# Performance work log

Measured on AMD Instinct MI355X. Metric: run time of the kernel, lower is better.

The kernel has to match this reference:

```python
import jax, jax.numpy as jnp
import numpy as np

CUTOFF = 10.0
EPS_W = 1e-5
EPS_LN = 1e-5

def _silu(v):
    return v * jax.nn.sigmoid(v)

def setup_inputs() -> dict:
    key = jax.random.key(0)
    ks = jax.random.split(key, 12)
    N, E, H, R = 50000, 300000, 256, 64
    s = lambda fan_in: 1.0 / np.sqrt(fan_in)
    inp = {
        'x': jax.random.normal(ks[0], (N, H), jnp.float32),
        'edge_index': jax.random.randint(ks[1], (2, E), 0, N, jnp.int64 if jax.config.jax_enable_x64 else jnp.int32),
        'distances': jax.random.uniform(ks[2], (E,), jnp.float32) * CUTOFF,
        'centers': jnp.linspace(0.0, CUTOFF, R).astype(jnp.float32),
        'widths': jnp.full((R,), CUTOFF / R, jnp.float32),
        'rbf_w1': jax.random.normal(ks[3], (R, R), jnp.float32) * s(R),
        'rbf_b1': jnp.zeros((R,), jnp.float32),
        'rbf_w2': jax.random.normal(ks[4], (R, R), jnp.float32) * s(R),
        'rbf_b2': jnp.zeros((R,), jnp.float32),
        'filt_w1': jax.random.normal(ks[5], (R, H), jnp.float32) * s(R),
        'filt_b1': jnp.zeros((H,), jnp.float32),
        'filt_w2': jax.random.normal(ks[6], (H, H), jnp.float32) * s(H),
        'filt_b2': jnp.zeros((H,), jnp.float32),
        'filt_w3': jax.random.normal(ks[7], (H, H), jnp.float32) * s(H),
        'filt_b3': jnp.zeros((H,), jnp.float32),
        'node_w': jax.random.normal(ks[8], (H, H), jnp.float32) * s(H),
        'node_b': jnp.zeros((H,), jnp.float32),
        'ln_g': jnp.ones((H,), jnp.float32),
        'ln_b': jnp.zeros((H,), jnp.float32),
        'gate_w': jax.random.normal(ks[9], (H, H), jnp.float32) * s(H),
        'gate_b': jnp.zeros((H,), jnp.float32),
    }
    return inp

def reference(x, edge_index, distances, centers, widths,
              rbf_w1, rbf_b1, rbf_w2, rbf_b2,
              filt_w1, filt_b1, filt_w2, filt_b2, filt_w3, filt_b3,
              node_w, node_b, ln_g, ln_b, gate_w, gate_b):
    # LearnableRBF: envelope * gaussian basis, then 2-layer SiLU proj
    d = distances
    env = 0.5 * (jnp.cos(d * jnp.pi / CUTOFF) + 1.0) * (d < CUTOFF).astype(x.dtype)  # [E]
    rbf = jnp.exp(-0.5 * ((d[:, None] - centers) / (jnp.abs(widths) + EPS_W)) ** 2)   # [E,R]
    r = rbf * env[:, None]
    r = _silu(r @ rbf_w1 + rbf_b1) @ rbf_w2 + rbf_b2                                  # [E,R]
    # filter network: Lin-SiLU-Lin-SiLU-Lin
    W = _silu(r @ filt_w1 + filt_b1)
    W = _silu(W @ filt_w2 + filt_b2) @ filt_w3 + filt_b3                              # [E,H]
    # gather -> modulate -> scatter-add (CFConv messaging)
    row, col = edge_index[0], edge_index[1]
    msg = (x[col] @ node_w + node_b) * W                                              # [E,H]
    agg = jax.ops.segment_sum(msg, row, num_segments=x.shape[0])                      # [N,H]
    h = x + agg
    mu = jnp.mean(h, axis=-1, keepdims=True)
    var = jnp.var(h, axis=-1, keepdims=True)
    out = (h - mu) / jnp.sqrt(var + EPS_LN) * ln_g + ln_b
    return out * jax.nn.sigmoid(out @ gate_w + gate_b)
```

## Files before the change

### kernel.cpp

```cpp
#include <hip/hip_runtime.h>
#include <hip/hip_bf16.h>
#include <math.h>

typedef __attribute__((ext_vector_type(8))) short bf16x8;
typedef __attribute__((ext_vector_type(4))) float f32x4;
typedef unsigned short ushort_t;

constexpr float F_CUTOFF = 10.0f;
constexpr float F_EPS_W  = 1e-5f;
constexpr float F_EPS_LN = 1e-5f;
constexpr float F_PI     = 3.14159265358979323846f;

__device__ __forceinline__ float silu_f(float v)   { return v / (1.0f + __expf(-v)); }
__device__ __forceinline__ float sigmoid_f(float v){ return 1.0f / (1.0f + __expf(-v)); }

__device__ __forceinline__ ushort_t f2bf(float f) {
    union { __hip_bfloat16 h; ushort_t u; } v; v.h = __float2bfloat16(f); return v.u;
}
__device__ __forceinline__ float bf2f(ushort_t u) {
    union { __hip_bfloat16 h; ushort_t u; } v; v.u = u; return __bfloat162float(v.h);
}

__device__ __forceinline__ float f4c(const float4& v, int q) {
    return q == 0 ? v.x : q == 1 ? v.y : q == 2 ? v.z : v.w;
}

__global__ void cvt_transpose_kernel(const float* __restrict__ in, ushort_t* __restrict__ out,
                                     int K, int N, int logK)
{
    int idx = blockIdx.x * 256 + threadIdx.x;
    if (idx >= K * N) return;
    int n = idx >> logK;
    int k = idx & (K - 1);
    out[idx] = f2bf(in[k * N + n]);
}

__global__ __launch_bounds__(256)
void gemm256_bf16_kernel(const float* __restrict__ A, const float* __restrict__ Wm,
                         const float* __restrict__ bias, ushort_t* __restrict__ out, int M)
{
    __shared__ float4 As4[64][64];
    const int t = threadIdx.x;
    const int row0 = blockIdx.x * 64;

    #pragma unroll
    for (int i = 0; i < 16; ++i) {
        int flat = t + i * 256;
        int r = flat >> 6, k4 = flat & 63;
        int row = row0 + r;
        float4 v = make_float4(0.f, 0.f, 0.f, 0.f);
        if (row < M) v = reinterpret_cast<const float4*>(A)[row * 64 + k4];
        As4[r][k4] = v;
    }
    __syncthreads();

    const int jt  = t & 31;
    const int et  = t >> 5;
    const int j04 = jt * 2;
    const int r0  = et * 8;

    float acc[8][8];
    #pragma unroll
    for (int r = 0; r < 8; ++r)
        #pragma unroll
        for (int c = 0; c < 8; ++c) acc[r][c] = 0.f;

    for (int k4 = 0; k4 < 64; ++k4) {
        float4 a4[8];
        #pragma unroll
        for (int r = 0; r < 8; ++r) a4[r] = As4[r0 + r][k4];
        #pragma unroll
        for (int q = 0; q < 4; ++q) {
            const int k = k4 * 4 + q;
            float4 b0 = reinterpret_cast<const float4*>(Wm)[k * 64 + j04];
            float4 b1 = reinterpret_cast<const float4*>(Wm)[k * 64 + j04 + 1];
            float bb[8] = {b0.x, b0.y, b0.z, b0.w, b1.x, b1.y, b1.z, b1.w};
            #pragma unroll
            for (int r = 0; r < 8; ++r) {
                float av = f4c(a4[r], q);
                #pragma unroll
                for (int c = 0; c < 8; ++c) acc[r][c] = fmaf(av, bb[c], acc[r][c]);
            }
        }
    }

    float4 bv0 = reinterpret_cast<const float4*>(bias)[j04];
    float4 bv1 = reinterpret_cast<const float4*>(bias)[j04 + 1];
    float bb[8] = {bv0.x, bv0.y, bv0.z, bv0.w, bv1.x, bv1.y, bv1.z, bv1.w};

    #pragma unroll
    for (int r = 0; r < 8; ++r) {
        int row = row0 + r0 + r;
        if (row >= M) continue;
        ushort_t o8[8];
        #pragma unroll
        for (int c = 0; c < 8; ++c) o8[c] = f2bf(acc[r][c] + bb[c]);
        *reinterpret_cast<uint4*>(out + (size_t)row * 256 + jt * 8) = *reinterpret_cast<uint4*>(o8);
    }
}

__global__ __launch_bounds__(256)
void gate_gemm_kernel(const float* __restrict__ A, const float* __restrict__ Wm,
                      const float* __restrict__ bias, float* __restrict__ out, int M)
{
    __shared__ float4 As4[64][64];
    const int t = threadIdx.x;
    const int row0 = blockIdx.x * 64;

    #pragma unroll
    for (int i = 0; i < 16; ++i) {
        int flat = t + i * 256;
        int r = flat >> 6, k4 = flat & 63;
        int row = row0 + r;
        float4 v = make_float4(0.f, 0.f, 0.f, 0.f);
        if (row < M) v = reinterpret_cast<const float4*>(A)[row * 64 + k4];
        As4[r][k4] = v;
    }
    __syncthreads();

    const int jt  = t & 31;
    const int et  = t >> 5;
    const int j04 = jt * 2;
    const int r0  = et * 8;

    float acc[8][8];
    #pragma unroll
    for (int r = 0; r < 8; ++r)
        #pragma unroll
        for (int c = 0; c < 8; ++c) acc[r][c] = 0.f;

    for (int k4 = 0; k4 < 64; ++k4) {
        float4 a4[8];
        #pragma unroll
        for (int r = 0; r < 8; ++r) a4[r] = As4[r0 + r][k4];
        #pragma unroll
        for (int q = 0; q < 4; ++q) {
            const int k = k4 * 4 + q;
            float4 b0 = reinterpret_cast<const float4*>(Wm)[k * 64 + j04];
            float4 b1 = reinterpret_cast<const float4*>(Wm)[k * 64 + j04 + 1];
            float bb[8] = {b0.x, b0.y, b0.z, b0.w, b1.x, b1.y, b1.z, b1.w};
            #pragma unroll
            for (int r = 0; r < 8; ++r) {
                float av = f4c(a4[r], q);
                #pragma unroll
                for (int c = 0; c < 8; ++c) acc[r][c] = fmaf(av, bb[c], acc[r][c]);
            }
        }
    }

    float4 bv0 = reinterpret_cast<const float4*>(bias)[j04];
    float4 bv1 = reinterpret_cast<const float4*>(bias)[j04 + 1];
    float bb[8] = {bv0.x, bv0.y, bv0.z, bv0.w, bv1.x, bv1.y, bv1.z, bv1.w};

    #pragma unroll
    for (int r = 0; r < 8; ++r) {
        int row = row0 + r0 + r;
        if (row >= M) continue;
        float4 a0 = As4[r0 + r][j04];
        float4 a1 = As4[r0 + r][j04 + 1];
        float aa[8] = {a0.x, a0.y, a0.z, a0.w, a1.x, a1.y, a1.z, a1.w};
        float o[8];
        #pragma unroll
        for (int c = 0; c < 8; ++c) o[c] = aa[c] * sigmoid_f(acc[r][c] + bb[c]);
        reinterpret_cast<float4*>(out)[row * 64 + j04]     = make_float4(o[0], o[1], o[2], o[3]);
        reinterpret_cast<float4*>(out)[row * 64 + j04 + 1] = make_float4(o[4], o[5], o[6], o[7]);
    }
}

template<int KS, int NT, bool SILU>
__device__ __forceinline__ void mlp_stage(const unsigned char* in, unsigned char* out,
                                          const ushort_t* __restrict__ Wt,
                                          const float* __restrict__ bias,
                                          int wm, int wn, int g, int q)
{
    constexpr int K = KS * 32;
    f32x4 acc[4][NT];
    #pragma unroll
    for (int mt = 0; mt < 4; ++mt)
        #pragma unroll
        for (int nt = 0; nt < NT; ++nt) acc[mt][nt] = (f32x4){0.f, 0.f, 0.f, 0.f};

    #pragma unroll
    for (int kk = 0; kk < KS; ++kk) {
        bf16x8 a[4];
        #pragma unroll
        for (int mt = 0; mt < 4; ++mt) {
            int m = wm * 64 + mt * 16 + q;
            int unit = (4 * kk + g) ^ (m & 7);
            a[mt] = *reinterpret_cast<const bf16x8*>(in + m * 512 + unit * 16);
        }
        bf16x8 b[NT];
        #pragma unroll
        for (int nt = 0; nt < NT; ++nt) {
            int n = (wn * NT + nt) * 16 + q;
            b[nt] = *reinterpret_cast<const bf16x8*>(Wt + n * K + kk * 32 + g * 8);
        }
        #pragma unroll
        for (int mt = 0; mt < 4; ++mt)
            #pragma unroll
            for (int nt = 0; nt < NT; ++nt)
                acc[mt][nt] = __builtin_amdgcn_mfma_f32_16x16x32_bf16(a[mt], b[nt], acc[mt][nt], 0, 0, 0);
    }

    const bool evenq = (q & 1) == 0;
    #pragma unroll
    for (int nt = 0; nt < NT; ++nt) {
        int n0  = (wn * NT + nt) * 16 + q;
        int n_e = n0 & ~1;
        float2 bv = *reinterpret_cast<const float2*>(bias + n_e);
        #pragma unroll
        for (int mt = 0; mt < 4; ++mt) {
            float v[4], p[4];
            #pragma unroll
            for (int r = 0; r < 4; ++r) { v[r] = acc[mt][nt][r]; p[r] = __shfl_xor(v[r], 1, 64); }
            #pragma unroll
            for (int rr = 0; rr < 2; ++rr) {
                int r = evenq ? rr : (2 + rr);
                float lo = (evenq ? v[r] : p[r]) + bv.x;
                float hi = (evenq ? p[r] : v[r]) + bv.y;
                if (SILU) { lo = silu_f(lo); hi = silu_f(hi); }
                int m = wm * 64 + mt * 16 + 4 * g + r;
                unsigned u = (unsigned)f2bf(lo) | ((unsigned)f2bf(hi) << 16);
                int byte = m * 512 + (((n_e >> 3) ^ (m & 7)) << 4) + ((n_e & 7) * 2);
                *reinterpret_cast<unsigned*>(out + byte) = u;
            }
        }
    }
}

__global__ __launch_bounds__(512)
void edge_mfma_kernel(const float* __restrict__ dist, const int* __restrict__ eidx,
                      const float* __restrict__ centers, const float* __restrict__ widths,
                      const ushort_t* __restrict__ wt_rbf1, const float* __restrict__ rbf_b1,
                      const ushort_t* __restrict__ wt_rbf2, const float* __restrict__ rbf_b2,
                      const ushort_t* __restrict__ wt_f1, const float* __restrict__ filt_b1,
                      const ushort_t* __restrict__ wt_f2, const float* __restrict__ filt_b2,
                      const ushort_t* __restrict__ wt_f3, const float* __restrict__ filt_b3,
                      const ushort_t* __restrict__ y, float* __restrict__ agg, int E)
{
    extern __shared__ __align__(16) unsigned char smem[];
    unsigned char* bufA = smem;
    unsigned char* bufB = smem + 65536;

    const int t  = threadIdx.x;
    const int e0 = blockIdx.x * 128;
    const int w    = t >> 6;
    const int wm   = w >> 2, wn = w & 3;
    const int lane = t & 63;
    const int g = lane >> 4, q = lane & 15;

    {
        int e  = t >> 2;
        int k0 = (t & 3) * 16;
        int ge = e0 + e;
        float d = (ge < E) ? dist[ge] : F_CUTOFF;
        float env = (d < F_CUTOFF) ? 0.5f * (__cosf(d * (F_PI / F_CUTOFF)) + 1.0f) : 0.0f;
        unsigned char* rowp = bufA + e * 512;
        #pragma unroll
        for (int i = 0; i < 8; ++i) {
            int n = k0 + 2 * i;
            float c0 = centers[n],     w0 = fabsf(widths[n]) + F_EPS_W;
            float c1 = centers[n + 1], w1 = fabsf(widths[n + 1]) + F_EPS_W;
            float z0 = (d - c0) / w0, z1 = (d - c1) / w1;
            float r0 = env * __expf(-0.5f * z0 * z0);
            float r1 = env * __expf(-0.5f * z1 * z1);
            unsigned u = (unsigned)f2bf(r0) | ((unsigned)f2bf(r1) << 16);
            int byte = (((n >> 3) ^ (e & 7)) << 4) + ((n & 7) * 2);
            *reinterpret_cast<unsigned*>(rowp + byte) = u;
        }
    }
    __syncthreads();

    mlp_stage<2, 1, true >(bufA, bufB, wt_rbf1, rbf_b1, wm, wn, g, q);
    __syncthreads();
    mlp_stage<2, 1, false>(bufB, bufA, wt_rbf2, rbf_b2, wm, wn, g, q);
    __syncthreads();
    mlp_stage<2, 4, true >(bufA, bufB, wt_f1, filt_b1, wm, wn, g, q);
    __syncthreads();
    mlp_stage<8, 4, true >(bufB, bufA, wt_f2, filt_b2, wm, wn, g, q);
    __syncthreads();

    {
        f32x4 acc[4][4];
        #pragma unroll
        for (int mt = 0; mt < 4; ++mt)
            #pragma unroll
            for (int nt = 0; nt < 4; ++nt) acc[mt][nt] = (f32x4){0.f, 0.f, 0.f, 0.f};

        #pragma unroll
        for (int kk = 0; kk < 8; ++kk) {
            bf16x8 a[4];
            #pragma unroll
            for (int mt = 0; mt < 4; ++mt) {
                int m = wm * 64 + mt * 16 + q;
                int unit = (4 * kk + g) ^ (m & 7);
                a[mt] = *reinterpret_cast<const bf16x8*>(bufA + m * 512 + unit * 16);
            }
            bf16x8 b[4];
            #pragma unroll
            for (int nt = 0; nt < 4; ++nt) {
                int n = (wn * 4 + nt) * 16 + q;
                b[nt] = *reinterpret_cast<const bf16x8*>(wt_f3 + n * 256 + kk * 32 + g * 8);
            }
            #pragma unroll
            for (int mt = 0; mt < 4; ++mt)
                #pragma unroll
                for (int nt = 0; nt < 4; ++nt)
                    acc[mt][nt] = __builtin_amdgcn_mfma_f32_16x16x32_bf16(a[mt], b[nt], acc[mt][nt], 0, 0, 0);
        }

        float bn[4];
        int   nn[4];
        #pragma unroll
        for (int nt = 0; nt < 4; ++nt) { nn[nt] = (wn * 4 + nt) * 16 + q; bn[nt] = filt_b3[nn[nt]]; }

        #pragma unroll
        for (int mt = 0; mt < 4; ++mt) {
            #pragma unroll
            for (int r = 0; r < 4; ++r) {
                int m  = wm * 64 + mt * 16 + 4 * g + r;
                int ge = e0 + m;
                if (ge < E) {
                    int rowi = eidx[ge];
                    int coli = eidx[E + ge];
                    const ushort_t* yrow = y + (size_t)coli * 256;
                    float* arow = agg + (size_t)rowi * 256;
                    #pragma unroll
                    for (int nt = 0; nt < 4; ++nt) {
                        float wv = acc[mt][nt][r] + bn[nt];
                        float yv = bf2f(yrow[nn[nt]]);
                        unsafeAtomicAdd(&arow[nn[nt]], wv * yv);
                    }
                }
            }
        }
    }
}

__global__ __launch_bounds__(256)
void ln_kernel(const float* __restrict__ x, const float* __restrict__ agg,
               const float* __restrict__ g, const float* __restrict__ b,
               float* __restrict__ out0, int N)
{
    int lane = threadIdx.x & 63;
    int row  = blockIdx.x * 4 + (threadIdx.x >> 6);
    if (row >= N) return;
    float4 hx = reinterpret_cast<const float4*>(x)[row * 64 + lane];
    float4 ha = reinterpret_cast<const float4*>(agg)[row * 64 + lane];
    float4 h  = make_float4(hx.x + ha.x, hx.y + ha.y, hx.z + ha.z, hx.w + ha.w);
    float s  = h.x + h.y + h.z + h.w;
    float s2 = h.x * h.x + h.y * h.y + h.z * h.z + h.w * h.w;
    #pragma unroll
    for (int off = 32; off > 0; off >>= 1) {
        s  += __shfl_xor(s,  off, 64);
        s2 += __shfl_xor(s2, off, 64);
    }
    float mu  = s * (1.0f / 256.0f);
    float var = s2 * (1.0f / 256.0f) - mu * mu;
    float inv = rsqrtf(var + F_EPS_LN);
    float4 gv = reinterpret_cast<const float4*>(g)[lane];
    float4 bv = reinterpret_cast<const float4*>(b)[lane];
    float4 o;
    o.x = (h.x - mu) * inv * gv.x + bv.x;
    o.y = (h.y - mu) * inv * gv.y + bv.y;
    o.z = (h.z - mu) * inv * gv.z + bv.z;
    o.w = (h.w - mu) * inv * gv.w + bv.w;
    reinterpret_cast<float4*>(out0)[row * 64 + lane] = o;
}

extern "C" void kernel_launch(void* const* d_in, const int* in_sizes, int n_in,
                              void* d_out, int out_size, void* d_ws, size_t ws_size,
                              hipStream_t stream)
{
    const float* x       = (const float*)d_in[0];
    const int*   eidx    = (const int*)  d_in[1];
    const float* dist    = (const float*)d_in[2];
    const float* centers = (const float*)d_in[3];
    const float* widths  = (const float*)d_in[4];
    const float* rbf_w1  = (const float*)d_in[5];
    const float* rbf_b1  = (const float*)d_in[6];
    const float* rbf_w2  = (const float*)d_in[7];
    const float* rbf_b2  = (const float*)d_in[8];
    const float* filt_w1 = (const float*)d_in[9];
    const float* filt_b1 = (const float*)d_in[10];
    const float* filt_w2 = (const float*)d_in[11];
    const float* filt_b2 = (const float*)d_in[12];
    const float* filt_w3 = (const float*)d_in[13];
    const float* filt_b3 = (const float*)d_in[14];
    const float* node_w  = (const float*)d_in[15];
    const float* node_b  = (const float*)d_in[16];
    const float* ln_g    = (const float*)d_in[17];
    const float* ln_b    = (const float*)d_in[18];
    const float* gate_w  = (const float*)d_in[19];
    const float* gate_b  = (const float*)d_in[20];

    const int N = in_sizes[0] / 256;
    const int E = in_sizes[2];

    ushort_t* y_bf = (ushort_t*)d_ws;
    ushort_t* wt1  = y_bf + (size_t)N * 256;
    ushort_t* wt2  = wt1 + 64 * 64;
    ushort_t* wf1  = wt2 + 64 * 64;
    ushort_t* wf2  = wf1 + 256 * 64;
    ushort_t* wf3  = wf2 + 256 * 256;

    float* agg = (float*)d_out;

    hipMemsetAsync(d_out, 0, (size_t)out_size * sizeof(float), stream);

    cvt_transpose_kernel<<<dim3((64 * 64 + 255) / 256),   256, 0, stream>>>(rbf_w1,  wt1, 64, 64, 6);
    cvt_transpose_kernel<<<dim3((64 * 64 + 255) / 256),   256, 0, stream>>>(rbf_w2,  wt2, 64, 64, 6);
    cvt_transpose_kernel<<<dim3((64 * 256 + 255) / 256),  256, 0, stream>>>(filt_w1, wf1, 64, 256, 6);
    cvt_transpose_kernel<<<dim3((256 * 256 + 255) / 256), 256, 0, stream>>>(filt_w2, wf2, 256, 256, 8);
    cvt_transpose_kernel<<<dim3((256 * 256 + 255) / 256), 256, 0, stream>>>(filt_w3, wf3, 256, 256, 8);

    gemm256_bf16_kernel<<<dim3((N + 63) / 64), 256, 0, stream>>>(x, node_w, node_b, y_bf, N);

    hipFuncSetAttribute((const void*)edge_mfma_kernel,
                        hipFuncAttributeMaxDynamicSharedMemorySize, 131072);
    edge_mfma_kernel<<<dim3((E + 127) / 128), 512, 131072, stream>>>(
        dist, eidx, centers, widths,
        wt1, rbf_b1, wt2, rbf_b2,
        wf1, filt_b1, wf2, filt_b2, wf3, filt_b3,
        y_bf, agg, E);

    ln_kernel<<<dim3((N + 3) / 4), 256, 0, stream>>>(x, agg, ln_g, ln_b, (float*)d_out, N);
    gate_gemm_kernel<<<dim3((N + 63) / 64), 256, 0, stream>>>((float*)d_out, gate_w, gate_b, (float*)d_out, N);
}
```

Baseline: 1.022 ms.

## Fold rbf_w2 into filt_w1 and halve edge tile for higher occupancy

Since the second RBF layer has no activation, its weight and bias are precomputed into the first filter layer (W2·Wf1, b2·Wf1+bf1) by small prep kernels. This removes one MFMA stage and one block-wide barrier per edge tile. The edge tile also shrinks from 128 to 64 edges, so shared memory drops to 64KB static with launch bounds requesting 4 blocks, aiming for more resident blocks to hide gather and atomic latency. The trade-off is that the fused weight is rounded to bf16 after combining, which changes rounding slightly, and each block now reuses the loaded weights over fewer edges.

Result: faster. 848.0 us (-17.1%).

```diff
diff --git a/kernel.cpp b/kernel.cpp
--- a/kernel.cpp
+++ b/kernel.cpp
@@ -33,6 +33,27 @@
     int n = idx >> logK;
     int k = idx & (K - 1);
     out[idx] = f2bf(in[k * N + n]);
+}
+
+__global__ void combine_w_kernel(const float* __restrict__ w2, const float* __restrict__ fw1,
+                                 ushort_t* __restrict__ out)
+{
+    int idx = blockIdx.x * 256 + threadIdx.x;
+    int c = idx >> 6, j = idx & 63;
+    float s = 0.f;
+    #pragma unroll 8
+    for (int n = 0; n < 64; ++n) s += w2[j * 64 + n] * fw1[n * 256 + c];
+    out[idx] = f2bf(s);
+}
+
+__global__ void combine_b_kernel(const float* __restrict__ b2, const float* __restrict__ fw1,
+                                 const float* __restrict__ fb1, float* __restrict__ out)
+{
+    int c = threadIdx.x;
+    float s = fb1[c];
+    #pragma unroll 8
+    for (int n = 0; n < 64; ++n) s += b2[n] * fw1[n * 256 + c];
+    out[c] = s;
 }
 
 __global__ __launch_bounds__(256)
@@ -174,29 +195,29 @@
                                           int wm, int wn, int g, int q)
 {
     constexpr int K = KS * 32;
-    f32x4 acc[4][NT];
-    #pragma unroll
-    for (int mt = 0; mt < 4; ++mt)
+    f32x4 acc[2][NT];
+    #pragma unroll
+    for (int mt = 0; mt < 2; ++mt)
         #pragma unroll
         for (int nt = 0; nt < NT; ++nt) acc[mt][nt] = (f32x4){0.f, 0.f, 0.f, 0.f};
 
     #pragma unroll
     for (int kk = 0; kk < KS; ++kk) {
-        bf16x8 a[4];
-        #pragma unroll
-        for (int mt = 0; mt < 4; ++mt) {
-            int m = wm * 64 + mt * 16 + q;
-            int unit = (4 * kk + g) ^ (m & 7);
-            a[mt] = *reinterpret_cast<const bf16x8*>(in + m * 512 + unit * 16);
-        }
         bf16x8 b[NT];
         #pragma unroll
         for (int nt = 0; nt < NT; ++nt) {
             int n = (wn * NT + nt) * 16 + q;
             b[nt] = *reinterpret_cast<const bf16x8*>(Wt + n * K + kk * 32 + g * 8);
         }
-        #pragma unroll
-        for (int mt = 0; mt < 4; ++mt)
+        bf16x8 a[2];
+        #pragma unroll
+        for (int mt = 0; mt < 2; ++mt) {
+            int m = wm * 32 + mt * 16 + q;
+            int unit = (4 * kk + g) ^ (m & 7);
+            a[mt] = *reinterpret_cast<const bf16x8*>(in + m * 512 + unit * 16);
+        }
+        #pragma unroll
+        for (int mt = 0; mt < 2; ++mt)
             #pragma unroll
             for (int nt = 0; nt < NT; ++nt)
                 acc[mt][nt] = __builtin_amdgcn_mfma_f32_16x16x32_bf16(a[mt], b[nt], acc[mt][nt], 0, 0, 0);
@@ -209,7 +230,7 @@
         int n_e = n0 & ~1;
         float2 bv = *reinterpret_cast<const float2*>(bias + n_e);
         #pragma unroll
-        for (int mt = 0; mt < 4; ++mt) {
+        for (int mt = 0; mt < 2; ++mt) {
             float v[4], p[4];
             #pragma unroll
             for (int r = 0; r < 4; ++r) { v[r] = acc[mt][nt][r]; p[r] = __shfl_xor(v[r], 1, 64); }
@@ -219,7 +240,7 @@
                 float lo = (evenq ? v[r] : p[r]) + bv.x;
                 float hi = (evenq ? p[r] : v[r]) + bv.y;
                 if (SILU) { lo = silu_f(lo); hi = silu_f(hi); }
-                int m = wm * 64 + mt * 16 + 4 * g + r;
+                int m = wm * 32 + mt * 16 + 4 * g + r;
                 unsigned u = (unsigned)f2bf(lo) | ((unsigned)f2bf(hi) << 16);
                 int byte = m * 512 + (((n_e >> 3) ^ (m & 7)) << 4) + ((n_e & 7) * 2);
                 *reinterpret_cast<unsigned*>(out + byte) = u;
@@ -228,36 +249,34 @@
     }
 }
 
-__global__ __launch_bounds__(512)
+__global__ __launch_bounds__(512, 4)
 void edge_mfma_kernel(const float* __restrict__ dist, const int* __restrict__ eidx,
                       const float* __restrict__ centers, const float* __restrict__ widths,
                       const ushort_t* __restrict__ wt_rbf1, const float* __restrict__ rbf_b1,
-                      const ushort_t* __restrict__ wt_rbf2, const float* __restrict__ rbf_b2,
-                      const ushort_t* __restrict__ wt_f1, const float* __restrict__ filt_b1,
+                      const ushort_t* __restrict__ wt_comb, const float* __restrict__ b_comb,
                       const ushort_t* __restrict__ wt_f2, const float* __restrict__ filt_b2,
                       const ushort_t* __restrict__ wt_f3, const float* __restrict__ filt_b3,
                       const ushort_t* __restrict__ y, float* __restrict__ agg, int E)
 {
-    extern __shared__ __align__(16) unsigned char smem[];
-    unsigned char* bufA = smem;
-    unsigned char* bufB = smem + 65536;
+    __shared__ __align__(16) unsigned char bufA[32768];
+    __shared__ __align__(16) unsigned char bufB[32768];
 
     const int t  = threadIdx.x;
-    const int e0 = blockIdx.x * 128;
+    const int e0 = blockIdx.x * 64;
     const int w    = t >> 6;
     const int wm   = w >> 2, wn = w & 3;
     const int lane = t & 63;
     const int g = lane >> 4, q = lane & 15;
 
     {
-        int e  = t >> 2;
-        int k0 = (t & 3) * 16;
+        int e  = t >> 3;
+        int k0 = (t & 7) * 8;
         int ge = e0 + e;
         float d = (ge < E) ? dist[ge] : F_CUTOFF;
         float env = (d < F_CUTOFF) ? 0.5f * (__cosf(d * (F_PI / F_CUTOFF)) + 1.0f) : 0.0f;
         unsigned char* rowp = bufA + e * 512;
         #pragma unroll
-        for (int i = 0; i < 8; ++i) {
+        for (int i = 0; i < 4; ++i) {
             int n = k0 + 2 * i;
             float c0 = centers[n],     w0 = fabsf(widths[n]) + F_EPS_W;
             float c1 = centers[n + 1], w1 = fabsf(widths[n + 1]) + F_EPS_W;
@@ -271,39 +290,37 @@
     }
     __syncthreads();
 
-    mlp_stage<2, 1, true >(bufA, bufB, wt_rbf1, rbf_b1, wm, wn, g, q);
-    __syncthreads();
-    mlp_stage<2, 1, false>(bufB, bufA, wt_rbf2, rbf_b2, wm, wn, g, q);
-    __syncthreads();
-    mlp_stage<2, 4, true >(bufA, bufB, wt_f1, filt_b1, wm, wn, g, q);
-    __syncthreads();
-    mlp_stage<8, 4, true >(bufB, bufA, wt_f2, filt_b2, wm, wn, g, q);
+    mlp_stage<2, 1, true>(bufA, bufB, wt_rbf1, rbf_b1, wm, wn, g, q);
+    __syncthreads();
+    mlp_stage<2, 4, true>(bufB, bufA, wt_comb, b_comb, wm, wn, g, q);
+    __syncthreads();
+    mlp_stage<8, 4, true>(bufA, bufB, wt_f2, filt_b2, wm, wn, g, q);
     __syncthreads();
 
     {
-        f32x4 acc[4][4];
-        #pragma unroll
-        for (int mt = 0; mt < 4; ++mt)
+        f32x4 acc[2][4];
+        #pragma unroll
+        for (int mt = 0; mt < 2; ++mt)
             #pragma unroll
             for (int nt = 0; nt < 4; ++nt) acc[mt][nt] = (f32x4){0.f, 0.f, 0.f, 0.f};
 
         #pragma unroll
         for (int kk = 0; kk < 8; ++kk) {
-            bf16x8 a[4];
-            #pragma unroll
-            for (int mt = 0; mt < 4; ++mt) {
-                int m = wm * 64 + mt * 16 + q;
-                int unit = (4 * kk + g) ^ (m & 7);
-                a[mt] = *reinterpret_cast<const bf16x8*>(bufA + m * 512 + unit * 16);
-            }
             bf16x8 b[4];
             #pragma unroll
             for (int nt = 0; nt < 4; ++nt) {
                 int n = (wn * 4 + nt) * 16 + q;
                 b[nt] = *reinterpret_cast<const bf16x8*>(wt_f3 + n * 256 + kk * 32 + g * 8);
             }
-            #pragma unroll
-            for (int mt = 0; mt < 4; ++mt)
+            bf16x8 a[2];
+            #pragma unroll
+            for (int mt = 0; mt < 2; ++mt) {
+                int m = wm * 32 + mt * 16 + q;
+                int unit = (4 * kk + g) ^ (m & 7);
+                a[mt] = *reinterpret_cast<const bf16x8*>(bufB + m * 512 + unit * 16);
+            }
+            #pragma unroll
+            for (int mt = 0; mt < 2; ++mt)
                 #pragma unroll
                 for (int nt = 0; nt < 4; ++nt)
                     acc[mt][nt] = __builtin_amdgcn_mfma_f32_16x16x32_bf16(a[mt], b[nt], acc[mt][nt], 0, 0, 0);
@@ -315,10 +332,10 @@
         for (int nt = 0; nt < 4; ++nt) { nn[nt] = (wn * 4 + nt) * 16 + q; bn[nt] = filt_b3[nn[nt]]; }
 
         #pragma unroll
-        for (int mt = 0; mt < 4; ++mt) {
+        for (int mt = 0; mt < 2; ++mt) {
             #pragma unroll
             for (int r = 0; r < 4; ++r) {
-                int m  = wm * 64 + mt * 16 + 4 * g + r;
+                int m  = wm * 32 + mt * 16 + 4 * g + r;
                 int ge = e0 + m;
                 if (ge < E) {
                     int rowi = eidx[ge];
@@ -397,31 +414,29 @@
     const int N = in_sizes[0] / 256;
     const int E = in_sizes[2];
 
-    ushort_t* y_bf = (ushort_t*)d_ws;
-    ushort_t* wt1  = y_bf + (size_t)N * 256;
-    ushort_t* wt2  = wt1 + 64 * 64;
-    ushort_t* wf1  = wt2 + 64 * 64;
-    ushort_t* wf2  = wf1 + 256 * 64;
-    ushort_t* wf3  = wf2 + 256 * 256;
+    ushort_t* y_bf   = (ushort_t*)d_ws;
+    ushort_t* wt1    = y_bf + (size_t)N * 256;
+    ushort_t* wcomb  = wt1 + 64 * 64;
+    ushort_t* wf2    = wcomb + 256 * 64;
+    ushort_t* wf3    = wf2 + 256 * 256;
+    float*    bcomb  = (float*)(wf3 + 256 * 256);
 
     float* agg = (float*)d_out;
 
     hipMemsetAsync(d_out, 0, (size_t)out_size * sizeof(float), stream);
 
     cvt_transpose_kernel<<<dim3((64 * 64 + 255) / 256),   256, 0, stream>>>(rbf_w1,  wt1, 64, 64, 6);
-    cvt_transpose_kernel<<<dim3((64 * 64 + 255) / 256),   256, 0, stream>>>(rbf_w2,  wt2, 64, 64, 6);
-    cvt_transpose_kernel<<<dim3((64 * 256 + 255) / 256),  256, 0, stream>>>(filt_w1, wf1, 64, 256, 6);
+    combine_w_kernel<<<dim3(64), 256, 0, stream>>>(rbf_w2, filt_w1, wcomb);
+    combine_b_kernel<<<dim3(1), 256, 0, stream>>>(rbf_b2, filt_w1, filt_b1, bcomb);
     cvt_transpose_kernel<<<dim3((256 * 256 + 255) / 256), 256, 0, stream>>>(filt_w2, wf2, 256, 256, 8);
     cvt_transpose_kernel<<<dim3((256 * 256 + 255) / 256), 256, 0, stream>>>(filt_w3, wf3, 256, 256, 8);
 
     gemm256_bf16_kernel<<<dim3((N + 63) / 64), 256, 0, stream>>>(x, node_w, node_b, y_bf, N);
 
-    hipFuncSetAttribute((const void*)edge_mfma_kernel,
-                        hipFuncAttributeMaxDynamicSharedMemorySize, 131072);
-    edge_mfma_kernel<<<dim3((E + 127) / 128), 512, 131072, stream>>>(
+    edge_mfma_kernel<<<dim3((E + 63) / 64), 512, 0, stream>>>(
         dist, eidx, centers, widths,
-        wt1, rbf_b1, wt2, rbf_b2,
-        wf1, filt_b1, wf2, filt_b2, wf3, filt_b3,
+        wt1, rbf_b1, wcomb, bcomb,
+        wf2, filt_b2, wf3, filt_b3,
         y_bf, agg, E);
 
     ln_kernel<<<dim3((N + 3) / 4), 256, 0, stream>>>(x, agg, ln_g, ln_b, (float*)d_out, N);
```
